# Kernel optimization log

Measured on AMD Instinct MI355X. Metric: run time of the kernel, lower is better.

Reference implementation:

```python
import jax, jax.numpy as jnp
import numpy as np

# Per-feature MLP topology from NAM._get_topology: 1->32->64->128->64->32->16->1
DIMS = [1, 32, 64, 128, 64, 32, 16, 1]
N_LAYERS = len(DIMS) - 1  # 7 linear layers
BATCH, DIM = 2048, 256


def setup_inputs() -> dict:
    key = jax.random.key(0)
    inp = {"x": jax.random.normal(jax.random.fold_in(key, 0), (BATCH, DIM), dtype=jnp.float32)}
    # Batched parameters: stack the `dim` independent tiny MLPs along a leading axis.
    # torch.nn.Linear default init: U(-1/sqrt(fan_in), 1/sqrt(fan_in)) for W and b.
    for l in range(N_LAYERS):
        fi, fo = DIMS[l], DIMS[l + 1]
        kw, kb = jax.random.split(jax.random.fold_in(key, l + 1))
        bound = 1.0 / np.sqrt(fi)
        inp[f"W{l}"] = jax.random.uniform(kw, (DIM, fi, fo), jnp.float32, -bound, bound)
        inp[f"b{l}"] = jax.random.uniform(kb, (DIM, fo), jnp.float32, -bound, bound)
    return inp


def reference(x, W0, b0, W1, b1, W2, b2, W3, b3, W4, b4, W5, b5, W6, b6):
    Ws = [W0, W1, W2, W3, W4, W5, W6]
    bs = [b0, b1, b2, b3, b4, b5, b6]
    # h: [batch, dim, feat] — all `dim` tiny MLPs run as one batched GEMM per layer
    h = x[:, :, None]
    for l in range(N_LAYERS):
        h = jnp.einsum('bdi,dio->bdo', h, Ws[l]) + bs[l][None, :, :]
        if l < N_LAYERS - 1:
            h = jax.nn.relu(h)
    # funcs_sum = sum over features of each per-feature scalar output -> [batch, 1]
    return jnp.sum(h, axis=1)
```

## Files before the change

kernel.cpp:

```cpp
#include <hip/hip_runtime.h>

#define BATCH 2048
#define DIM   256

typedef _Float16 half8 __attribute__((ext_vector_type(8)));
typedef _Float16 half4 __attribute__((ext_vector_type(4)));
typedef __attribute__((ext_vector_type(4))) float f32x4;

#define NTILES 41
#define TILE_HALVES 1024
#define PACK_OFF_BYTES (BATCH * DIM * 4)

template <int FI, int FO, int BASE>
__device__ __forceinline__ void prep_layer(const float* __restrict__ W, int d,
                                           int t, _Float16* __restrict__ pack) {
  constexpr int KT = FI / 32, NT = FO / 16, T = KT * NT;
  const float* Wd = W + (size_t)d * FI * FO;
  for (int job = t; job < T * 64; job += 256) {
    const int tile = job >> 6, lane = job & 63;
    const int m = lane & 15, q = lane >> 4;
    const int nt = tile / KT, kt = tile % KT;
    const float* Wp = Wd + (size_t)(kt * 32 + q * 8) * FO + nt * 16 + m;
    half8 hi, lo;
#pragma unroll
    for (int j = 0; j < 8; ++j) {
      const float w = Wp[(size_t)j * FO];
      const _Float16 h = (_Float16)w;
      hi[j] = h;
      lo[j] = (_Float16)(w - (float)h);
    }
    _Float16* base = pack + (size_t)(d * NTILES + BASE + tile) * TILE_HALVES;
    *(half8*)(base + lane * 8) = hi;
    *(half8*)(base + 512 + lane * 8) = lo;
  }
}

__global__ __launch_bounds__(256) void prep_kernel(
    const float* __restrict__ W1, const float* __restrict__ W2,
    const float* __restrict__ W3, const float* __restrict__ W4,
    const float* __restrict__ W5, _Float16* __restrict__ pack) {
  const int d = blockIdx.x, t = threadIdx.x;
  switch (blockIdx.y) {
    case 0: prep_layer<32, 64, 0>(W1, d, t, pack); break;
    case 1: prep_layer<64, 128, 4>(W2, d, t, pack); break;
    case 2: prep_layer<128, 64, 20>(W3, d, t, pack); break;
    case 3: prep_layer<64, 32, 36>(W4, d, t, pack); break;
    default: prep_layer<32, 16, 40>(W5, d, t, pack); break;
  }
}

template <int FI, int FO, int LBASE, bool EXTRACT>
__device__ __forceinline__ void layer_mfma(
    const _Float16* __restrict__ packd, const float* __restrict__ bld,
    int m, int q, int lane, _Float16* __restrict__ bw,
    const half8 (*A)[4], half8 (*O)[4]) {
  constexpr int KT = FI / 32, NT = FO / 16;
#pragma unroll
  for (int nt = 0; nt < NT; ++nt) {
    const float bias = bld[nt * 16 + m];
    f32x4 acc[4];
#pragma unroll
    for (int rt = 0; rt < 4; ++rt) acc[rt] = {bias, bias, bias, bias};
#pragma unroll
    for (int kt = 0; kt < KT; ++kt) {
      const _Float16* tb = packd + (size_t)(LBASE + nt * KT + kt) * TILE_HALVES;
      const half8 Bh = *(const half8*)(tb + lane * 8);
      const half8 Bl = *(const half8*)(tb + 512 + lane * 8);
#pragma unroll
      for (int rt = 0; rt < 4; ++rt) {
        acc[rt] = __builtin_amdgcn_mfma_f32_16x16x32_f16(A[rt][kt], Bh, acc[rt], 0, 0, 0);
        acc[rt] = __builtin_amdgcn_mfma_f32_16x16x32_f16(A[rt][kt], Bl, acc[rt], 0, 0, 0);
      }
    }
    const int hcol = (nt & 1) * 16 + m;
#pragma unroll
    for (int rt = 0; rt < 4; ++rt)
#pragma unroll
      for (int r = 0; r < 4; ++r)
        bw[rt * 576 + (q * 4 + r) * 36 + hcol] =
            (_Float16)fmaxf(acc[rt][r], 0.0f);
    if (EXTRACT && (nt & 1)) {
      const int ktn = nt >> 1;
#pragma unroll
      for (int rt = 0; rt < 4; ++rt) {
        const _Float16* p = &bw[rt * 576 + m * 36 + q * 8];
        const half4 v0 = *(const half4*)p;
        const half4 v1 = *(const half4*)(p + 4);
        half8 o;
#pragma unroll
        for (int j = 0; j < 4; ++j) { o[j] = v0[j]; o[4 + j] = v1[j]; }
        O[rt][ktn] = o;
      }
    }
  }
}

__global__ __launch_bounds__(256, 1) void mlp_mfma(
    const float* __restrict__ x,
    const float* __restrict__ W0, const float* __restrict__ b0,
    const float* __restrict__ b1, const float* __restrict__ b2,
    const float* __restrict__ b3, const float* __restrict__ b4,
    const float* __restrict__ b5,
    const float* __restrict__ W6, const float* __restrict__ b6,
    const _Float16* __restrict__ pack, float* __restrict__ partial) {
  const int lane = threadIdx.x & 63;
  const int wave = threadIdx.x >> 6;
  const int m = lane & 15, q = lane >> 4;
  const int d = blockIdx.x;
  const int row0 = blockIdx.y * 256 + wave * 64;

  __shared__ __align__(16) _Float16 buf[4][4 * 576];
  _Float16* bw = buf[wave];
  const _Float16* packd = pack + (size_t)d * NTILES * TILE_HALVES;

  half8 A0[4][4], A1[4][4];

#pragma unroll
  for (int rt = 0; rt < 4; ++rt) {
    const float xv = x[(size_t)(row0 + rt * 16 + m) * DIM + d];
    half8 h;
#pragma unroll
    for (int j = 0; j < 8; ++j)
      h[j] = (_Float16)fmaxf(
          fmaf(xv, W0[d * 32 + q * 8 + j], b0[d * 32 + q * 8 + j]), 0.0f);
    A0[rt][0] = h;
  }

  layer_mfma<32, 64, 0, true>(packd, b1 + d * 64, m, q, lane, bw, A0, A1);
  layer_mfma<64, 128, 4, true>(packd, b2 + d * 128, m, q, lane, bw, A1, A0);
  layer_mfma<128, 64, 20, true>(packd, b3 + d * 64, m, q, lane, bw, A0, A1);
  layer_mfma<64, 32, 36, true>(packd, b4 + d * 32, m, q, lane, bw, A1, A0);
  layer_mfma<32, 16, 40, false>(packd, b5 + d * 16, m, q, lane, bw, A0, A1);

  {
    const float w6 = W6[d * 16 + m];
    const float bias6 = b6[d];
#pragma unroll
    for (int rt = 0; rt < 4; ++rt) {
#pragma unroll
      for (int r = 0; r < 4; ++r) {
        float v = (float)bw[rt * 576 + (q * 4 + r) * 36 + m] * w6;
        v += __shfl_xor(v, 1);
        v += __shfl_xor(v, 2);
        v += __shfl_xor(v, 4);
        v += __shfl_xor(v, 8);
        if (m == 0)
          partial[(size_t)d * BATCH + row0 + rt * 16 + q * 4 + r] = v + bias6;
      }
    }
  }
}

__global__ __launch_bounds__(256) void reduce_kernel(
    const float* __restrict__ partial, float* __restrict__ out) {
  const int b = blockIdx.x * blockDim.x + threadIdx.x;
  float s = 0.0f;
#pragma unroll 8
  for (int d = 0; d < DIM; ++d) s += partial[(size_t)d * BATCH + b];
  out[b] = s;
}

extern "C" void kernel_launch(void* const* d_in, const int* in_sizes, int n_in,
                              void* d_out, int out_size, void* d_ws, size_t ws_size,
                              hipStream_t stream) {
  const float* x = (const float*)d_in[0];
  const float* W[7];
  const float* B[7];
  for (int l = 0; l < 7; ++l) {
    W[l] = (const float*)d_in[1 + 2 * l];
    B[l] = (const float*)d_in[2 + 2 * l];
  }
  float* partial = (float*)d_ws;
  _Float16* pack = (_Float16*)((char*)d_ws + PACK_OFF_BYTES);

  prep_kernel<<<dim3(DIM, 5), dim3(256), 0, stream>>>(W[1], W[2], W[3], W[4],
                                                      W[5], pack);

  mlp_mfma<<<dim3(DIM, BATCH / 256), dim3(256), 0, stream>>>(
      x, W[0], B[0], B[1], B[2], B[3], B[4], B[5], W[6], B[6], pack, partial);

  reduce_kernel<<<dim3(BATCH / 256), dim3(256), 0, stream>>>(partial,
                                                             (float*)d_out);
}
```

Baseline: 158.7 us.

## Fuse weight packing into MLP kernel and stage packed weights in LDS

```diff
diff --git a/kernel.cpp b/kernel.cpp
--- a/kernel.cpp
+++ b/kernel.cpp
@@ -2,6 +2,7 @@
 
 #define BATCH 2048
 #define DIM   256
+#define WAVES 8
 
 typedef _Float16 half8 __attribute__((ext_vector_type(8)));
 typedef _Float16 half4 __attribute__((ext_vector_type(4)));
@@ -9,49 +10,11 @@
 
 #define NTILES 41
 #define TILE_HALVES 1024
-#define PACK_OFF_BYTES (BATCH * DIM * 4)
-
-template <int FI, int FO, int BASE>
-__device__ __forceinline__ void prep_layer(const float* __restrict__ W, int d,
-                                           int t, _Float16* __restrict__ pack) {
-  constexpr int KT = FI / 32, NT = FO / 16, T = KT * NT;
-  const float* Wd = W + (size_t)d * FI * FO;
-  for (int job = t; job < T * 64; job += 256) {
-    const int tile = job >> 6, lane = job & 63;
-    const int m = lane & 15, q = lane >> 4;
-    const int nt = tile / KT, kt = tile % KT;
-    const float* Wp = Wd + (size_t)(kt * 32 + q * 8) * FO + nt * 16 + m;
-    half8 hi, lo;
-#pragma unroll
-    for (int j = 0; j < 8; ++j) {
-      const float w = Wp[(size_t)j * FO];
-      const _Float16 h = (_Float16)w;
-      hi[j] = h;
-      lo[j] = (_Float16)(w - (float)h);
-    }
-    _Float16* base = pack + (size_t)(d * NTILES + BASE + tile) * TILE_HALVES;
-    *(half8*)(base + lane * 8) = hi;
-    *(half8*)(base + 512 + lane * 8) = lo;
-  }
-}
-
-__global__ __launch_bounds__(256) void prep_kernel(
-    const float* __restrict__ W1, const float* __restrict__ W2,
-    const float* __restrict__ W3, const float* __restrict__ W4,
-    const float* __restrict__ W5, _Float16* __restrict__ pack) {
-  const int d = blockIdx.x, t = threadIdx.x;
-  switch (blockIdx.y) {
-    case 0: prep_layer<32, 64, 0>(W1, d, t, pack); break;
-    case 1: prep_layer<64, 128, 4>(W2, d, t, pack); break;
-    case 2: prep_layer<128, 64, 20>(W3, d, t, pack); break;
-    case 3: prep_layer<64, 32, 36>(W4, d, t, pack); break;
-    default: prep_layer<32, 16, 40>(W5, d, t, pack); break;
-  }
-}
 
 template <int FI, int FO, int LBASE, bool EXTRACT>
 __device__ __forceinline__ void layer_mfma(
-    const _Float16* __restrict__ packd, const float* __restrict__ bld,
+    const _Float16* __restrict__ packs,
+    const float* __restrict__ bld,
     int m, int q, int lane, _Float16* __restrict__ bw,
     const half8 (*A)[4], half8 (*O)[4]) {
   constexpr int KT = FI / 32, NT = FO / 16;
@@ -63,7 +26,7 @@
     for (int rt = 0; rt < 4; ++rt) acc[rt] = {bias, bias, bias, bias};
 #pragma unroll
     for (int kt = 0; kt < KT; ++kt) {
-      const _Float16* tb = packd + (size_t)(LBASE + nt * KT + kt) * TILE_HALVES;
+      const _Float16* tb = packs + (size_t)(LBASE + nt * KT + kt) * TILE_HALVES;
       const half8 Bh = *(const half8*)(tb + lane * 8);
       const half8 Bl = *(const half8*)(tb + 512 + lane * 8);
 #pragma unroll
@@ -95,46 +58,84 @@
   }
 }
 
-__global__ __launch_bounds__(256, 1) void mlp_mfma(
+__global__ __launch_bounds__(512, 2) void mlp_fused(
     const float* __restrict__ x,
     const float* __restrict__ W0, const float* __restrict__ b0,
-    const float* __restrict__ b1, const float* __restrict__ b2,
-    const float* __restrict__ b3, const float* __restrict__ b4,
-    const float* __restrict__ b5,
+    const float* __restrict__ W1, const float* __restrict__ b1,
+    const float* __restrict__ W2, const float* __restrict__ b2,
+    const float* __restrict__ W3, const float* __restrict__ b3,
+    const float* __restrict__ W4, const float* __restrict__ b4,
+    const float* __restrict__ W5, const float* __restrict__ b5,
     const float* __restrict__ W6, const float* __restrict__ b6,
-    const _Float16* __restrict__ pack, float* __restrict__ partial) {
-  const int lane = threadIdx.x & 63;
-  const int wave = threadIdx.x >> 6;
+    float* __restrict__ partial) {
+  const int t = threadIdx.x;
+  const int lane = t & 63;
+  const int wave = t >> 6;
   const int m = lane & 15, q = lane >> 4;
   const int d = blockIdx.x;
-  const int row0 = blockIdx.y * 256 + wave * 64;
 
-  __shared__ __align__(16) _Float16 buf[4][4 * 576];
-  _Float16* bw = buf[wave];
-  const _Float16* packd = pack + (size_t)d * NTILES * TILE_HALVES;
+  __shared__ __align__(16) _Float16 packs[NTILES * TILE_HALVES];
+  __shared__ __align__(16) _Float16 act[WAVES][4 * 576];
 
+  for (int job = t; job < NTILES * 64; job += 512) {
+    const int tile = job >> 6, jl = job & 63;
+    const int jm = jl & 15, jq = jl >> 4;
+    const float* W; int FI, FO, lt;
+    if (tile < 4)       { W = W1; FI = 32;  FO = 64;  lt = tile; }
+    else if (tile < 20) { W = W2; FI = 64;  FO = 128; lt = tile - 4; }
+    else if (tile < 36) { W = W3; FI = 128; FO = 64;  lt = tile - 20; }
+    else if (tile < 40) { W = W4; FI = 64;  FO = 32;  lt = tile - 36; }
+    else                { W = W5; FI = 32;  FO = 16;  lt = 0; }
+    const int KT = FI >> 5;
+    const int nt = lt / KT, kt = lt - nt * KT;
+    const float* Wp = W + (size_t)d * FI * FO +
+                      (size_t)(kt * 32 + jq * 8) * FO + nt * 16 + jm;
+    half8 hi, lo;
+#pragma unroll
+    for (int j = 0; j < 8; ++j) {
+      const float w = Wp[(size_t)j * FO];
+      const _Float16 h = (_Float16)w;
+      hi[j] = h;
+      lo[j] = (_Float16)(w - (float)h);
+    }
+    _Float16* base = packs + (size_t)tile * TILE_HALVES;
+    *(half8*)(base + jl * 8) = hi;
+    *(half8*)(base + 512 + jl * 8) = lo;
+  }
+
+  float w0r[8], b0r[8];
+#pragma unroll
+  for (int j = 0; j < 8; ++j) {
+    w0r[j] = W0[d * 32 + q * 8 + j];
+    b0r[j] = b0[d * 32 + q * 8 + j];
+  }
+  const float w6 = W6[d * 16 + m];
+  const float bias6 = b6[d];
+
+  __syncthreads();
+
+  _Float16* bw = act[wave];
   half8 A0[4][4], A1[4][4];
 
+  for (int it = 0; it < 4; ++it) {
+    const int row0 = it * 512 + wave * 64;
+
 #pragma unroll
-  for (int rt = 0; rt < 4; ++rt) {
-    const float xv = x[(size_t)(row0 + rt * 16 + m) * DIM + d];
-    half8 h;
+    for (int rt = 0; rt < 4; ++rt) {
+      const float xv = x[(size_t)(row0 + rt * 16 + m) * DIM + d];
+      half8 h;
 #pragma unroll
-    for (int j = 0; j < 8; ++j)
-      h[j] = (_Float16)fmaxf(
-          fmaf(xv, W0[d * 32 + q * 8 + j], b0[d * 32 + q * 8 + j]), 0.0f);
-    A0[rt][0] = h;
-  }
+      for (int j = 0; j < 8; ++j)
+        h[j] = (_Float16)fmaxf(fmaf(xv, w0r[j], b0r[j]), 0.0f);
+      A0[rt][0] = h;
+    }
 
-  layer_mfma<32, 64, 0, true>(packd, b1 + d * 64, m, q, lane, bw, A0, A1);
-  layer_mfma<64, 128, 4, true>(packd, b2 + d * 128, m, q, lane, bw, A1, A0);
-  layer_mfma<128, 64, 20, true>(packd, b3 + d * 64, m, q, lane, bw, A0, A1);
-  layer_mfma<64, 32, 36, true>(packd, b4 + d * 32, m, q, lane, bw, A1, A0);
-  layer_mfma<32, 16, 40, false>(packd, b5 + d * 16, m, q, lane, bw, A0, A1);
+    layer_mfma<32, 64, 0, true>(packs, b1 + d * 64, m, q, lane, bw, A0, A1);
+    layer_mfma<64, 128, 4, true>(packs, b2 + d * 128, m, q, lane, bw, A1, A0);
+    layer_mfma<128, 64, 20, true>(packs, b3 + d * 64, m, q, lane, bw, A0, A1);
+    layer_mfma<64, 32, 36, true>(packs, b4 + d * 32, m, q, lane, bw, A1, A0);
+    layer_mfma<32, 16, 40, false>(packs, b5 + d * 16, m, q, lane, bw, A0, A1);
 
-  {
-    const float w6 = W6[d * 16 + m];
-    const float bias6 = b6[d];
 #pragma unroll
     for (int rt = 0; rt < 4; ++rt) {
 #pragma unroll
@@ -171,13 +172,10 @@
     B[l] = (const float*)d_in[2 + 2 * l];
   }
   float* partial = (float*)d_ws;
-  _Float16* pack = (_Float16*)((char*)d_ws + PACK_OFF_BYTES);
 
-  prep_kernel<<<dim3(DIM, 5), dim3(256), 0, stream>>>(W[1], W[2], W[3], W[4],
-                                                      W[5], pack);
-
-  mlp_mfma<<<dim3(DIM, BATCH / 256), dim3(256), 0, stream>>>(
-      x, W[0], B[0], B[1], B[2], B[3], B[4], B[5], W[6], B[6], pack, partial);
+  mlp_fused<<<dim3(DIM), dim3(512), 0, stream>>>(
+      x, W[0], B[0], W[1], B[1], W[2], B[2], W[3], B[3], W[4], B[4], W[5], B[5],
+      W[6], B[6], partial);
 
   reduce_kernel<<<dim3(BATCH / 256), dim3(256), 0, stream>>>(partial,
                                                              (float*)d_out);
```

Result: no change. 157.3 us (-0.9%).
